# Kernel optimization log

Measured on AMD Instinct MI355X. Metric: run time of the kernel, lower is better.

The kernel has to match this reference:

```python
import jax, jax.numpy as jnp
import numpy as np

N = 50000      # nodes
E = 800000     # edges (before self-loops)
F_IN = 128     # num_node_features
H = 128        # hidden_channels
G = 256        # graphs in batch
T = 4          # num_tasks


def setup_inputs() -> dict:
    key = jax.random.key(0)
    ks = jax.random.split(key, 12)
    x = jax.random.normal(ks[0], (N, F_IN), jnp.float32)
    edge_index = jax.random.randint(ks[1], (2, E), 0, N, dtype=jnp.int64)
    batch = jnp.sort(jax.random.randint(ks[2], (N,), 0, G, dtype=jnp.int64))
    s_in = 1.0 / np.sqrt(F_IN)
    s_h = 1.0 / np.sqrt(H)
    W1 = jax.random.normal(ks[3], (F_IN, H), jnp.float32) * s_in
    b1 = jnp.zeros((H,), jnp.float32)
    W2 = jax.random.normal(ks[4], (H, H), jnp.float32) * s_h
    b2 = jnp.zeros((H,), jnp.float32)
    Wfc = jax.random.normal(ks[5], (H, H), jnp.float32) * s_h
    bfc = jnp.zeros((H,), jnp.float32)
    Wh = jax.random.normal(ks[6], (T, H, 2), jnp.float32) * s_h
    bh = jnp.zeros((T, 2), jnp.float32)
    return {"x": x, "edge_index": edge_index, "batch": batch,
            "W1": W1, "b1": b1, "W2": W2, "b2": b2,
            "Wfc": Wfc, "bfc": bfc, "Wh": Wh, "bh": bh}


def _gcn_layer(x, W, b, src, dst, dinv):
    # GCNConv: out = D^{-1/2}(A+I)D^{-1/2} X W + b  (self-loops already in src/dst)
    h = x @ W                                    # [N, H] dense transform first (fewer edge features)
    coef = dinv[src] * dinv[dst]                 # [E+N] symmetric normalization
    msg = h[src] * coef[:, None]                 # [E+N, H] gathered messages
    out = jax.ops.segment_sum(msg, dst, num_segments=N)
    return out + b


def reference(x, edge_index, batch, W1, b1, W2, b2, Wfc, bfc, Wh, bh):
    loops = jnp.arange(N, dtype=edge_index.dtype)
    src = jnp.concatenate([edge_index[0], loops])  # [E+N]
    dst = jnp.concatenate([edge_index[1], loops])
    deg = jax.ops.segment_sum(jnp.ones_like(dst, dtype=x.dtype), dst, num_segments=N)
    dinv = jax.lax.rsqrt(deg)                      # deg >= 1 due to self-loops

    h = jax.nn.relu(_gcn_layer(x, W1, b1, src, dst, dinv))
    h = jax.nn.relu(_gcn_layer(h, W2, b2, src, dst, dinv))

    # global_mean_pool over batch ids
    sums = jax.ops.segment_sum(h, batch, num_segments=G)          # [G, H]
    cnt = jax.ops.segment_sum(jnp.ones((N,), h.dtype), batch, num_segments=G)
    pooled = sums / jnp.maximum(cnt, 1.0)[:, None]

    z = jax.nn.relu(pooled @ Wfc + bfc)                           # [G, H]
    out = jnp.einsum('gh,thc->tgc', z, Wh) + bh[:, None, :]       # [T, G, 2]
    return out
```

## Files before the change

### kernel.cpp

```cpp
#include <hip/hip_runtime.h>
#include <math.h>

constexpr int N = 50000;
constexpr int E = 800000;
constexpr int F = 128;
constexpr int G = 256;
constexpr int T = 4;

constexpr int BSH   = 5;
constexpr int BNODES= 1 << BSH;
constexpr int NBUCK = (N + BNODES - 1) / BNODES;
constexpr int CHUNK = 2048;
constexpr int NCHUNK= (E + CHUNK - 1) / CHUNK;
constexpr int SSH   = 13;

constexpr int WC_BLKS  = (F * F + 255) / 256;
constexpr int PRE_Z0   = 2 * WC_BLKS;
constexpr int PRE_ZB   = (G * F + 255) / 256;
constexpr int PRE_H0   = PRE_Z0 + PRE_ZB;
constexpr int PRE_BLKS = PRE_H0 + NCHUNK;

constexpr int GB1 = (N + 63) / 64;
constexpr int GCB = GB1 + NBUCK;
constexpr int AGB = N / 16;

typedef __attribute__((ext_vector_type(8))) short short8;
typedef __attribute__((ext_vector_type(4))) float floatx4;

__device__ inline float bf2f(unsigned short u) {
    union { unsigned int i; float f; } v;
    v.i = ((unsigned int)u) << 16;
    return v.f;
}
__device__ inline unsigned short f2bf(float f) {
    union { float f; unsigned int i; } v;
    v.f = f;
    unsigned int r = v.i + 0x7FFF + ((v.i >> 16) & 1);
    return (unsigned short)(r >> 16);
}
__device__ inline unsigned int pack2bf(float a, float b) {
    return (unsigned int)f2bf(a) | ((unsigned int)f2bf(b) << 16);
}

__device__ inline void wcast_one(const float* __restrict__ W,
                                 unsigned short* __restrict__ Whi,
                                 unsigned short* __restrict__ Wlo, int i) {
    if (i >= F * F) return;
    int k = i >> 7, n = i & 127;
    float w = W[i];
    unsigned short hi = f2bf(w);
    unsigned short lo = f2bf(w - bf2f(hi));
    int s = k >> 5, q = (k >> 3) & 3, j = k & 7;
    int idx = (((s * 128 + n) * 4 + q) * 8) + j;
    Whi[idx] = hi;
    Wlo[idx] = lo;
}

__global__ __launch_bounds__(256) void k_pre(const float* __restrict__ W1, const float* __restrict__ W2,
                                             unsigned short* __restrict__ w1h, unsigned short* __restrict__ w1l,
                                             unsigned short* __restrict__ w2h, unsigned short* __restrict__ w2l,
                                             const int* __restrict__ dst, int* __restrict__ cnts,
                                             float* __restrict__ pooled) {
    __shared__ int h[NBUCK];
    int b = blockIdx.x, t = threadIdx.x;
    if (b < WC_BLKS) {
        wcast_one(W1, w1h, w1l, b * 256 + t);
    } else if (b < 2 * WC_BLKS) {
        wcast_one(W2, w2h, w2l, (b - WC_BLKS) * 256 + t);
    } else if (b < PRE_H0) {
        pooled[(b - PRE_Z0) * 256 + t] = 0.f;
    } else {
        int chunk = b - PRE_H0;
        for (int i = t; i < NBUCK; i += 256) h[i] = 0;
        __syncthreads();
        int base = chunk * CHUNK;
        for (int i = t; i < CHUNK; i += 256) {
            int e = base + i;
            if (e < E) atomicAdd(&h[dst[e] >> BSH], 1);
        }
        __syncthreads();
        for (int i = t; i < NBUCK; i += 256) cnts[chunk * NBUCK + i] = h[i];
    }
}

__global__ __launch_bounds__(256) void k_bucketscan(const int* __restrict__ btot,
                                                    int* __restrict__ bucketbase) {
    __shared__ int part[256];
    int t = threadIdx.x;
    constexpr int CH = (NBUCK + 255) / 256;
    int beg = t * CH;
    int end = (beg + CH < NBUCK) ? beg + CH : NBUCK;
    int tot[CH];
    int s = 0;
    for (int i = beg; i < end; ++i) {
        tot[i - beg] = btot[i];
        s += btot[i];
    }
    part[t] = s;
    __syncthreads();
    for (int off = 1; off < 256; off <<= 1) {
        int u = (t >= off) ? part[t - off] : 0;
        __syncthreads();
        part[t] += u;
        __syncthreads();
    }
    int run = (t == 0) ? 0 : part[t - 1];
    for (int i = beg; i < end; ++i) {
        bucketbase[i] = run;
        run += tot[i - beg];
    }
    if (t == 255) bucketbase[NBUCK] = part[255];
}

__global__ __launch_bounds__(256) void k_fillb(const int* __restrict__ src,
                                               const int* __restrict__ dst,
                                               const int* __restrict__ cnts,
                                               const int* __restrict__ bucketbase,
                                               unsigned int* __restrict__ staging) {
    __shared__ int lofs[NBUCK];
    int chunk = blockIdx.x, t = threadIdx.x;
    for (int i = t; i < NBUCK; i += 256)
        lofs[i] = bucketbase[i] + cnts[chunk * NBUCK + i];
    __syncthreads();
    int base = chunk * CHUNK;
    for (int i = t; i < CHUNK; i += 256) {
        int e = base + i;
        if (e < E) {
            int d = dst[e];
            int pos = atomicAdd(&lofs[d >> BSH], 1);
            staging[pos] = (unsigned int)src[e] | ((unsigned int)(d & (BNODES - 1)) << 16);
        }
    }
}

__global__ __launch_bounds__(256) void k_passB(const unsigned int* __restrict__ staging,
                                               const int* __restrict__ bucketbase,
                                               int* __restrict__ csr,
                                               int* __restrict__ rowstart,
                                               float* __restrict__ dinv) {
    __shared__ unsigned int ent[1024];
    __shared__ int h[BNODES * 8], off_a[BNODES * 8];
    __shared__ int nodebase[BNODES], ndeg[BNODES];
    int b = blockIdx.x, t = threadIdx.x;
    int jb = bucketbase[b], je = bucketbase[b + 1];
    int M = je - jb;
    if (M > 1024) M = 1024;
    if (t < BNODES * 8) h[t] = 0;
    __syncthreads();

    for (int i = t; i < M; i += 256) {
        unsigned int en = staging[jb + i];
        ent[i] = en;
        int key = (((en >> 16) & (BNODES - 1)) << 3) | ((en & 0xFFFFu) >> SSH);
        atomicAdd(&h[key], 1);
    }
    __syncthreads();

    if (t < BNODES) {
        int s = 0;
#pragma unroll
        for (int c = 0; c < 8; ++c) s += h[t * 8 + c];
        ndeg[t] = s;
    }
    __syncthreads();
    if (t == 0) {
        int run = jb;
        for (int k = 0; k < BNODES; ++k) {
            nodebase[k] = run;
            run += ndeg[k];
        }
    }
    __syncthreads();
    if (t < BNODES) {
        int run = nodebase[t];
#pragma unroll
        for (int c = 0; c < 8; ++c) {
            off_a[t * 8 + c] = run;
            run += h[t * 8 + c];
        }
        int node = b * BNODES + t;
        if (node < N) {
            rowstart[node] = nodebase[t];
            dinv[node] = rsqrtf((float)(ndeg[t] + 1));
        }
    }
    if (b == 0 && t == 0) rowstart[N] = E;
    __syncthreads();

    for (int i = t; i < M; i += 256) {
        unsigned int en = ent[i];
        int key = (((en >> 16) & (BNODES - 1)) << 3) | ((en & 0xFFFFu) >> SSH);
        int loc = atomicAdd(&off_a[key], 1);
        csr[loc] = (int)(en & 0xFFFFu);
    }
}

template <bool ABF16>
__device__ __forceinline__ void gemm_body(const void* __restrict__ Ain,
                                          const unsigned short* __restrict__ Wph,
                                          const unsigned short* __restrict__ Wpl,
                                          unsigned short* __restrict__ C16,
                                          int row0, int tid,
                                          unsigned short* __restrict__ Albs) {
    if (ABF16) {
        const uint4* A8 = (const uint4*)Ain;
        for (int f = tid; f < 64 * 16; f += 256) {
            int r = f >> 4, kq = f & 15;
            int row = row0 + r;
            uint4 v = make_uint4(0u, 0u, 0u, 0u);
            if (row < N) v = A8[row * 16 + kq];
            *(uint4*)&Albs[r * 136 + kq * 8] = v;
        }
    } else {
        const float4* A4 = (const float4*)Ain;
        for (int f = tid; f < 64 * 32; f += 256) {
            int r = f >> 5, kq = f & 31;
            int row = row0 + r;
            float4 v = make_float4(0.f, 0.f, 0.f, 0.f);
            if (row < N) v = A4[row * 32 + kq];
            ushort4 o;
            o.x = f2bf(v.x); o.y = f2bf(v.y); o.z = f2bf(v.z); o.w = f2bf(v.w);
            *(ushort4*)&Albs[r * 136 + kq * 4] = o;
        }
    }
    __syncthreads();

    int wv = tid >> 6;
    int lane = tid & 63;
    int c16 = lane & 15;
    int q = lane >> 4;
    int m = wv * 16 + c16;

    floatx4 acc[8];
#pragma unroll
    for (int nt = 0; nt < 8; ++nt) acc[nt] = (floatx4){0.f, 0.f, 0.f, 0.f};

    const short8* WH = (const short8*)Wph;
    const short8* WL = (const short8*)Wpl;
#pragma unroll
    for (int s = 0; s < 4; ++s) {
        short8 a = *(const short8*)&Albs[m * 136 + s * 32 + q * 8];
        int wb = s * 512 + c16 * 4 + q;
#pragma unroll
        for (int nt = 0; nt < 8; ++nt) {
            acc[nt] = __builtin_amdgcn_mfma_f32_16x16x32_bf16(a, WH[wb + nt * 64], acc[nt], 0, 0, 0);
            acc[nt] = __builtin_amdgcn_mfma_f32_16x16x32_bf16(a, WL[wb + nt * 64], acc[nt], 0, 0, 0);
        }
    }

    int rbase = row0 + wv * 16 + q * 4;
#pragma unroll
    for (int r = 0; r < 4; ++r) {
        int row = rbase + r;
        if (row < N) {
#pragma unroll
            for (int nt = 0; nt < 8; ++nt)
                C16[row * 128 + nt * 16 + c16] = f2bf(acc[nt][r]);
        }
    }
}

__global__ __launch_bounds__(256) void k_gemmcol(const float* __restrict__ x,
                                                 const unsigned short* __restrict__ w1h,
                                                 const unsigned short* __restrict__ w1l,
                                                 unsigned short* __restrict__ tmp16,
                                                 int* __restrict__ cnts,
                                                 int* __restrict__ btot) {
    __shared__ __align__(16) unsigned short Albs[64 * 136];
    int b = blockIdx.x, t = threadIdx.x;
    if (b < GB1) {
        gemm_body<false>(x, w1h, w1l, tmp16, b * 64, t, Albs);
        return;
    }
    int j = b - GB1;
    int* part = (int*)Albs;
    int k0 = 2 * t, k1 = 2 * t + 1;
    int v0 = (k0 < NCHUNK) ? cnts[k0 * NBUCK + j] : 0;
    int v1 = (k1 < NCHUNK) ? cnts[k1 * NBUCK + j] : 0;
    int s = v0 + v1;
    part[t] = s;
    __syncthreads();
    for (int off = 1; off < 256; off <<= 1) {
        int u = (t >= off) ? part[t - off] : 0;
        __syncthreads();
        part[t] += u;
        __syncthreads();
    }
    int excl = part[t] - s;
    if (k0 < NCHUNK) cnts[k0 * NBUCK + j] = excl;
    if (k1 < NCHUNK) cnts[k1 * NBUCK + j] = excl + v0;
    if (t == 255) btot[j] = part[255];
}

__device__ inline void fma8(const uint4& u, float c, float* acc) {
    union { unsigned int i; float f; } a;
    a.i = u.x << 16;          acc[0] = fmaf(a.f, c, acc[0]);
    a.i = u.x & 0xFFFF0000u;  acc[1] = fmaf(a.f, c, acc[1]);
    a.i = u.y << 16;          acc[2] = fmaf(a.f, c, acc[2]);
    a.i = u.y & 0xFFFF0000u;  acc[3] = fmaf(a.f, c, acc[3]);
    a.i = u.z << 16;          acc[4] = fmaf(a.f, c, acc[4]);
    a.i = u.z & 0xFFFF0000u;  acc[5] = fmaf(a.f, c, acc[5]);
    a.i = u.w << 16;          acc[6] = fmaf(a.f, c, acc[6]);
    a.i = u.w & 0xFFFF0000u;  acc[7] = fmaf(a.f, c, acc[7]);
}

__device__ __forceinline__ void agg_loop(const uint4* __restrict__ t8,
                                         const int* __restrict__ csr,
                                         const float* __restrict__ dinv,
                                         int jb, int je, int lane, float* acc) {
    for (int j = jb; j < je; j += 8) {
        int e[8];
        float cf[8];
#pragma unroll
        for (int k = 0; k < 8; ++k) {
            int idx = j + k;
            e[k] = csr[idx < je ? idx : je - 1];
            cf[k] = (idx < je) ? dinv[e[k]] : 0.0f;
        }
        uint4 u[8];
#pragma unroll
        for (int k = 0; k < 8; ++k) u[k] = t8[e[k] * 16 + lane];
#pragma unroll
        for (int k = 0; k < 8; ++k) fma8(u[k], cf[k], acc);
    }
}

__global__ __launch_bounds__(256) void k_agg1gemm(const unsigned short* __restrict__ tmp16,
                                                  const int* __restrict__ csr,
                                                  const int* __restrict__ rowstart,
                                                  const float* __restrict__ dinv,
                                                  const float* __restrict__ bias,
                                                  const unsigned short* __restrict__ w2h,
                                                  const unsigned short* __restrict__ w2l,
                                                  unsigned short* __restrict__ tmp2) {
    __shared__ __align__(16) unsigned short Albs[16 * 136];
    int tid = threadIdx.x;
    int row0 = blockIdx.x * 16;

    {
        int node = row0 + (tid >> 4);
        int lane = tid & 15;
        const uint4* t8 = (const uint4*)tmp16;
        float di = dinv[node];
        float acc[8] = {0.f, 0.f, 0.f, 0.f, 0.f, 0.f, 0.f, 0.f};
        fma8(t8[node * 16 + lane], di, acc);
        agg_loop(t8, csr, dinv, rowstart[node], rowstart[node + 1], lane, acc);

        const float4* b4 = (const float4*)bias;
        float4 ba = b4[lane * 2], bb = b4[lane * 2 + 1];
        uint4 o;
        o.x = pack2bf(fmaxf(fmaf(acc[0], di, ba.x), 0.f), fmaxf(fmaf(acc[1], di, ba.y), 0.f));
        o.y = pack2bf(fmaxf(fmaf(acc[2], di, ba.z), 0.f), fmaxf(fmaf(acc[3], di, ba.w), 0.f));
        o.z = pack2bf(fmaxf(fmaf(acc[4], di, bb.x), 0.f), fmaxf(fmaf(acc[5], di, bb.y), 0.f));
        o.w = pack2bf(fmaxf(fmaf(acc[6], di, bb.z), 0.f), fmaxf(fmaf(acc[7], di, bb.w), 0.f));
        *(uint4*)&Albs[(tid >> 4) * 136 + lane * 8] = o;
    }
    __syncthreads();

    int wv = tid >> 6;
    int lane = tid & 63;
    int c16 = lane & 15;
    int q = lane >> 4;

    floatx4 acc[2];
    acc[0] = (floatx4){0.f, 0.f, 0.f, 0.f};
    acc[1] = (floatx4){0.f, 0.f, 0.f, 0.f};

    const short8* WH = (const short8*)w2h;
    const short8* WL = (const short8*)w2l;
#pragma unroll
    for (int s = 0; s < 4; ++s) {
        short8 a = *(const short8*)&Albs[c16 * 136 + s * 32 + q * 8];
        int wb = s * 512 + c16 * 4 + q;
#pragma unroll
        for (int i = 0; i < 2; ++i) {
            int nt = wv * 2 + i;
            acc[i] = __builtin_amdgcn_mfma_f32_16x16x32_bf16(a, WH[wb + nt * 64], acc[i], 0, 0, 0);
            acc[i] = __builtin_amdgcn_mfma_f32_16x16x32_bf16(a, WL[wb + nt * 64], acc[i], 0, 0, 0);
        }
    }

    int rbase = row0 + q * 4;
#pragma unroll
    for (int r = 0; r < 4; ++r) {
        int row = rbase + r;
#pragma unroll
        for (int i = 0; i < 2; ++i) {
            int nt = wv * 2 + i;
            tmp2[row * 128 + nt * 16 + c16] = f2bf(acc[i][r]);
        }
    }
}

__global__ __launch_bounds__(256) void k_agg(const unsigned short* __restrict__ tmp16,
                                             const int* __restrict__ csr,
                                             const int* __restrict__ rowstart,
                                             const float* __restrict__ dinv,
                                             const float* __restrict__ bias,
                                             const int* __restrict__ batch,
                                             float* __restrict__ pooled) {
    __shared__ float red[16][128];
    __shared__ int gid[16];
    int tid = threadIdx.x;
    int node0 = blockIdx.x * 16;
    int ns = tid >> 4, lane = tid & 15;
    int node = node0 + ns;
    const uint4* t8 = (const uint4*)tmp16;
    float di = dinv[node];
    float acc[8] = {0.f, 0.f, 0.f, 0.f, 0.f, 0.f, 0.f, 0.f};
    fma8(t8[node * 16 + lane], di, acc);
    agg_loop(t8, csr, dinv, rowstart[node], rowstart[node + 1], lane, acc);

    const float4* b4 = (const float4*)bias;
    float4 ba = b4[lane * 2], bb = b4[lane * 2 + 1];
    red[ns][lane * 8 + 0] = fmaxf(fmaf(acc[0], di, ba.x), 0.f);
    red[ns][lane * 8 + 1] = fmaxf(fmaf(acc[1], di, ba.y), 0.f);
    red[ns][lane * 8 + 2] = fmaxf(fmaf(acc[2], di, ba.z), 0.f);
    red[ns][lane * 8 + 3] = fmaxf(fmaf(acc[3], di, ba.w), 0.f);
    red[ns][lane * 8 + 4] = fmaxf(fmaf(acc[4], di, bb.x), 0.f);
    red[ns][lane * 8 + 5] = fmaxf(fmaf(acc[5], di, bb.y), 0.f);
    red[ns][lane * 8 + 6] = fmaxf(fmaf(acc[6], di, bb.z), 0.f);
    red[ns][lane * 8 + 7] = fmaxf(fmaf(acc[7], di, bb.w), 0.f);
    if (tid < 16) gid[tid] = batch[node0 + tid];
    __syncthreads();

    if (tid < 128) {
        int f = tid;
        float run = 0.f;
        int g = gid[0];
        for (int r = 0; r < 16; ++r) {
            if (gid[r] != g) {
                atomicAdd(&pooled[g * 128 + f], run);
                run = 0.f;
                g = gid[r];
            }
            run += red[r][f];
        }
        atomicAdd(&pooled[g * 128 + f], run);
    }
}

__global__ __launch_bounds__(128) void k_poolhead(const float* __restrict__ pooled,
                                                  const int* __restrict__ batch,
                                                  const float* __restrict__ Wfc,
                                                  const float* __restrict__ bfc,
                                                  const float* __restrict__ Wh,
                                                  const float* __restrict__ bh,
                                                  float* __restrict__ out) {
    __shared__ float p[128];
    __shared__ float zs[128];
    int g = blockIdx.x, t = threadIdx.x;

    int lo = 0, hi = N;
    while (lo < hi) { int m = (lo + hi) >> 1; if (batch[m] < g) lo = m + 1; else hi = m; }
    int lo1 = lo, hi1 = N;
    while (lo1 < hi1) { int m = (lo1 + hi1) >> 1; if (batch[m] < g + 1) lo1 = m + 1; else hi1 = m; }
    int cnt = lo1 - lo;
    float inv = 1.0f / (float)((cnt > 1) ? cnt : 1);

    p[t] = pooled[g * 128 + t] * inv;
    __syncthreads();

    float a = bfc[t];
    for (int k = 0; k < F; ++k) a = fmaf(p[k], Wfc[k * F + t], a);
    zs[t] = fmaxf(a, 0.f);
    __syncthreads();

    if (t < T * 2) {
        int task = t >> 1, c = t & 1;
        float a2 = bh[task * 2 + c];
        const float* wr = &Wh[task * F * 2 + c];
        for (int h = 0; h < F; ++h) a2 = fmaf(zs[h], wr[h * 2], a2);
        out[task * (G * 2) + g * 2 + c] = a2;
    }
}

extern "C" void kernel_launch(void* const* d_in, const int* in_sizes, int n_in,
                              void* d_out, int out_size, void* d_ws, size_t ws_size,
                              hipStream_t stream) {
    const float* x    = (const float*)d_in[0];
    const int*   ei   = (const int*)d_in[1];
    const int*   batch= (const int*)d_in[2];
    const float* W1   = (const float*)d_in[3];
    const float* b1   = (const float*)d_in[4];
    const float* W2   = (const float*)d_in[5];
    const float* b2   = (const float*)d_in[6];
    const float* Wfc  = (const float*)d_in[7];
    const float* bfc  = (const float*)d_in[8];
    const float* Wh   = (const float*)d_in[9];
    const float* bh   = (const float*)d_in[10];
    float* out = (float*)d_out;

    const int* srcp = ei;
    const int* dstp = ei + E;

    char* w = (char*)d_ws;
    auto alloc = [&](size_t bytes) {
        char* p = w;
        w += (bytes + 255) & ~(size_t)255;
        return p;
    };
    unsigned short* tmp16 = (unsigned short*)alloc((size_t)N * F * 2);
    unsigned short* tmp2  = (unsigned short*)alloc((size_t)N * F * 2);
    int*   csr      = (int*)  alloc((size_t)E * 4);
    unsigned int* staging = (unsigned int*)alloc((size_t)E * 4);
    int*   cnts     = (int*)  alloc((size_t)NCHUNK * NBUCK * 4);
    int*   btot     = (int*)  alloc((size_t)NBUCK * 4);
    int*   bucketbase=(int*)  alloc((size_t)(NBUCK + 1) * 4);
    int*   rowstart = (int*)  alloc((size_t)(N + 1) * 4);
    float* dinv     = (float*)alloc((size_t)N * 4);
    float* pooled   = (float*)alloc((size_t)G * F * 4);
    unsigned short* w1h = (unsigned short*)alloc((size_t)F * F * 2);
    unsigned short* w1l = (unsigned short*)alloc((size_t)F * F * 2);
    unsigned short* w2h = (unsigned short*)alloc((size_t)F * F * 2);
    unsigned short* w2l = (unsigned short*)alloc((size_t)F * F * 2);

    k_pre<<<PRE_BLKS, 256, 0, stream>>>(W1, W2, w1h, w1l, w2h, w2l, dstp, cnts, pooled);

    k_gemmcol<<<GCB, 256, 0, stream>>>(x, w1h, w1l, tmp16, cnts, btot);

    k_bucketscan<<<1, 256, 0, stream>>>(btot, bucketbase);
    k_fillb<<<NCHUNK, 256, 0, stream>>>(srcp, dstp, cnts, bucketbase, staging);
    k_passB<<<NBUCK, 256, 0, stream>>>(staging, bucketbase, csr, rowstart, dinv);

    k_agg1gemm<<<AGB, 256, 0, stream>>>(tmp16, csr, rowstart, dinv, b1, w2h, w2l, tmp2);

    k_agg<<<AGB, 256, 0, stream>>>(tmp2, csr, rowstart, dinv, b2, batch, pooled);

    k_poolhead<<<G, 128, 0, stream>>>(pooled, batch, Wfc, bfc, Wh, bh, out);
}
```

Before: 232.0 us.

## Prescale GEMM outputs by dinv, fuse bucket scan into fill, pipeline CSR loads

Per-node in-degree is now counted with global atomics in the pre-pass. That lets dinv be computed inside the first GEMM epilogue, and each transformed row is stored already multiplied by dinv[src]. The aggregation loops then sum rows with plain adds instead of gathering dinv per edge, and the second GEMM likewise prescales its output. The single-block bucket scan kernel is folded into every fill block, removing one launch at the cost of redundant scans. The aggregation loop also prefetches the next group of CSR indices. The new global atomics and memset add some cost.

```diff
diff --git a/kernel.cpp b/kernel.cpp
--- a/kernel.cpp
+++ b/kernel.cpp
@@ -60,7 +60,7 @@
                                              unsigned short* __restrict__ w1h, unsigned short* __restrict__ w1l,
                                              unsigned short* __restrict__ w2h, unsigned short* __restrict__ w2l,
                                              const int* __restrict__ dst, int* __restrict__ cnts,
-                                             float* __restrict__ pooled) {
+                                             float* __restrict__ pooled, int* __restrict__ ndeg) {
     __shared__ int h[NBUCK];
     int b = blockIdx.x, t = threadIdx.x;
     if (b < WC_BLKS) {
@@ -76,17 +76,28 @@
         int base = chunk * CHUNK;
         for (int i = t; i < CHUNK; i += 256) {
             int e = base + i;
-            if (e < E) atomicAdd(&h[dst[e] >> BSH], 1);
+            if (e < E) {
+                int d = dst[e];
+                atomicAdd(&h[d >> BSH], 1);
+                atomicAdd(&ndeg[d], 1);
+            }
         }
         __syncthreads();
         for (int i = t; i < NBUCK; i += 256) cnts[chunk * NBUCK + i] = h[i];
     }
 }
 
-__global__ __launch_bounds__(256) void k_bucketscan(const int* __restrict__ btot,
-                                                    int* __restrict__ bucketbase) {
+__global__ __launch_bounds__(256) void k_fillb(const int* __restrict__ src,
+                                               const int* __restrict__ dst,
+                                               const int* __restrict__ cnts,
+                                               const int* __restrict__ btot,
+                                               int* __restrict__ bucketbase,
+                                               unsigned int* __restrict__ staging) {
+    __shared__ int bb[NBUCK + 1];
     __shared__ int part[256];
-    int t = threadIdx.x;
+    __shared__ int lofs[NBUCK];
+    int chunk = blockIdx.x, t = threadIdx.x;
+
     constexpr int CH = (NBUCK + 255) / 256;
     int beg = t * CH;
     int end = (beg + CH < NBUCK) ? beg + CH : NBUCK;
@@ -106,22 +117,18 @@
     }
     int run = (t == 0) ? 0 : part[t - 1];
     for (int i = beg; i < end; ++i) {
-        bucketbase[i] = run;
+        bb[i] = run;
         run += tot[i - beg];
     }
-    if (t == 255) bucketbase[NBUCK] = part[255];
-}
-
-__global__ __launch_bounds__(256) void k_fillb(const int* __restrict__ src,
-                                               const int* __restrict__ dst,
-                                               const int* __restrict__ cnts,
-                                               const int* __restrict__ bucketbase,
-                                               unsigned int* __restrict__ staging) {
-    __shared__ int lofs[NBUCK];
-    int chunk = blockIdx.x, t = threadIdx.x;
+    if (t == 255) bb[NBUCK] = part[255];
+    __syncthreads();
+    if (chunk == 0)
+        for (int i = t; i <= NBUCK; i += 256) bucketbase[i] = bb[i];
+
     for (int i = t; i < NBUCK; i += 256)
-        lofs[i] = bucketbase[i] + cnts[chunk * NBUCK + i];
-    __syncthreads();
+        lofs[i] = bb[i] + cnts[chunk * NBUCK + i];
+    __syncthreads();
+
     int base = chunk * CHUNK;
     for (int i = t; i < CHUNK; i += 256) {
         int e = base + i;
@@ -136,8 +143,7 @@
 __global__ __launch_bounds__(256) void k_passB(const unsigned int* __restrict__ staging,
                                                const int* __restrict__ bucketbase,
                                                int* __restrict__ csr,
-                                               int* __restrict__ rowstart,
-                                               float* __restrict__ dinv) {
+                                               int* __restrict__ rowstart) {
     __shared__ unsigned int ent[1024];
     __shared__ int h[BNODES * 8], off_a[BNODES * 8];
     __shared__ int nodebase[BNODES], ndeg[BNODES];
@@ -179,10 +185,7 @@
             run += h[t * 8 + c];
         }
         int node = b * BNODES + t;
-        if (node < N) {
-            rowstart[node] = nodebase[t];
-            dinv[node] = rsqrtf((float)(ndeg[t] + 1));
-        }
+        if (node < N) rowstart[node] = nodebase[t];
     }
     if (b == 0 && t == 0) rowstart[N] = E;
     __syncthreads();
@@ -199,6 +202,8 @@
 __device__ __forceinline__ void gemm_body(const void* __restrict__ Ain,
                                           const unsigned short* __restrict__ Wph,
                                           const unsigned short* __restrict__ Wpl,
+                                          const int* __restrict__ ndeg,
+                                          float* __restrict__ dinvout,
                                           unsigned short* __restrict__ C16,
                                           int row0, int tid,
                                           unsigned short* __restrict__ Albs) {
@@ -253,9 +258,11 @@
     for (int r = 0; r < 4; ++r) {
         int row = rbase + r;
         if (row < N) {
+            float dv = rsqrtf((float)(ndeg[row] + 1));
+            if (c16 == 0) dinvout[row] = dv;
 #pragma unroll
             for (int nt = 0; nt < 8; ++nt)
-                C16[row * 128 + nt * 16 + c16] = f2bf(acc[nt][r]);
+                C16[row * 128 + nt * 16 + c16] = f2bf(acc[nt][r] * dv);
         }
     }
 }
@@ -263,13 +270,15 @@
 __global__ __launch_bounds__(256) void k_gemmcol(const float* __restrict__ x,
                                                  const unsigned short* __restrict__ w1h,
                                                  const unsigned short* __restrict__ w1l,
+                                                 const int* __restrict__ ndeg,
+                                                 float* __restrict__ dinv,
                                                  unsigned short* __restrict__ tmp16,
                                                  int* __restrict__ cnts,
                                                  int* __restrict__ btot) {
     __shared__ __align__(16) unsigned short Albs[64 * 136];
     int b = blockIdx.x, t = threadIdx.x;
     if (b < GB1) {
-        gemm_body<false>(x, w1h, w1l, tmp16, b * 64, t, Albs);
+        gemm_body<false>(x, w1h, w1l, ndeg, dinv, tmp16, b * 64, t, Albs);
         return;
     }
     int j = b - GB1;
@@ -290,6 +299,18 @@
     if (k0 < NCHUNK) cnts[k0 * NBUCK + j] = excl;
     if (k1 < NCHUNK) cnts[k1 * NBUCK + j] = excl + v0;
     if (t == 255) btot[j] = part[255];
+}
+
+__device__ inline void add8(const uint4& u, float* acc) {
+    union { unsigned int i; float f; } a;
+    a.i = u.x << 16;          acc[0] += a.f;
+    a.i = u.x & 0xFFFF0000u;  acc[1] += a.f;
+    a.i = u.y << 16;          acc[2] += a.f;
+    a.i = u.y & 0xFFFF0000u;  acc[3] += a.f;
+    a.i = u.z << 16;          acc[4] += a.f;
+    a.i = u.z & 0xFFFF0000u;  acc[5] += a.f;
+    a.i = u.w << 16;          acc[6] += a.f;
+    a.i = u.w & 0xFFFF0000u;  acc[7] += a.f;
 }
 
 __device__ inline void fma8(const uint4& u, float c, float* acc) {
@@ -304,24 +325,42 @@
     a.i = u.w & 0xFFFF0000u;  acc[7] = fmaf(a.f, c, acc[7]);
 }
 
-__device__ __forceinline__ void agg_loop(const uint4* __restrict__ t8,
+__device__ __forceinline__ void agg_loop(const uint4* __restrict__ t8l,
                                          const int* __restrict__ csr,
-                                         const float* __restrict__ dinv,
-                                         int jb, int je, int lane, float* acc) {
-    for (int j = jb; j < je; j += 8) {
+                                         int jb, int je, float* acc) {
+    int n8 = (je - jb) >> 3;
+    int j = jb;
+    if (n8 > 0) {
         int e[8];
-        float cf[8];
+#pragma unroll
+        for (int k = 0; k < 8; ++k) e[k] = csr[j + k];
+        for (int c = 0; c < n8; ++c) {
+            uint4 u[8];
+#pragma unroll
+            for (int k = 0; k < 8; ++k) u[k] = t8l[e[k] * 16];
+            j += 8;
+            if (c + 1 < n8) {
+#pragma unroll
+                for (int k = 0; k < 8; ++k) e[k] = csr[j + k];
+            }
+#pragma unroll
+            for (int k = 0; k < 8; ++k) add8(u[k], acc);
+        }
+    }
+    if (j < je) {
+        int e[8];
+        float msk[8];
 #pragma unroll
         for (int k = 0; k < 8; ++k) {
             int idx = j + k;
             e[k] = csr[idx < je ? idx : je - 1];
-            cf[k] = (idx < je) ? dinv[e[k]] : 0.0f;
+            msk[k] = (idx < je) ? 1.0f : 0.0f;
         }
         uint4 u[8];
 #pragma unroll
-        for (int k = 0; k < 8; ++k) u[k] = t8[e[k] * 16 + lane];
-#pragma unroll
-        for (int k = 0; k < 8; ++k) fma8(u[k], cf[k], acc);
+        for (int k = 0; k < 8; ++k) u[k] = t8l[e[k] * 16];
+#pragma unroll
+        for (int k = 0; k < 8; ++k) fma8(u[k], msk[k], acc);
     }
 }
 
@@ -340,12 +379,12 @@
     {
         int node = row0 + (tid >> 4);
         int lane = tid & 15;
-        const uint4* t8 = (const uint4*)tmp16;
+        const uint4* t8l = (const uint4*)tmp16 + lane;
+        float acc[8] = {0.f, 0.f, 0.f, 0.f, 0.f, 0.f, 0.f, 0.f};
+        add8(t8l[node * 16], acc);
+        agg_loop(t8l, csr, rowstart[node], rowstart[node + 1], acc);
+
         float di = dinv[node];
-        float acc[8] = {0.f, 0.f, 0.f, 0.f, 0.f, 0.f, 0.f, 0.f};
-        fma8(t8[node * 16 + lane], di, acc);
-        agg_loop(t8, csr, dinv, rowstart[node], rowstart[node + 1], lane, acc);
-
         const float4* b4 = (const float4*)bias;
         float4 ba = b4[lane * 2], bb = b4[lane * 2 + 1];
         uint4 o;
@@ -384,10 +423,11 @@
 #pragma unroll
     for (int r = 0; r < 4; ++r) {
         int row = rbase + r;
+        float dv = dinv[row];
 #pragma unroll
         for (int i = 0; i < 2; ++i) {
             int nt = wv * 2 + i;
-            tmp2[row * 128 + nt * 16 + c16] = f2bf(acc[i][r]);
+            tmp2[row * 128 + nt * 16 + c16] = f2bf(acc[i][r] * dv);
         }
     }
 }
@@ -405,12 +445,12 @@
     int node0 = blockIdx.x * 16;
     int ns = tid >> 4, lane = tid & 15;
     int node = node0 + ns;
-    const uint4* t8 = (const uint4*)tmp16;
+    const uint4* t8l = (const uint4*)tmp16 + lane;
+    float acc[8] = {0.f, 0.f, 0.f, 0.f, 0.f, 0.f, 0.f, 0.f};
+    add8(t8l[node * 16], acc);
+    agg_loop(t8l, csr, rowstart[node], rowstart[node + 1], acc);
+
     float di = dinv[node];
-    float acc[8] = {0.f, 0.f, 0.f, 0.f, 0.f, 0.f, 0.f, 0.f};
-    fma8(t8[node * 16 + lane], di, acc);
-    agg_loop(t8, csr, dinv, rowstart[node], rowstart[node + 1], lane, acc);
-
     const float4* b4 = (const float4*)bias;
     float4 ba = b4[lane * 2], bb = b4[lane * 2 + 1];
     red[ns][lane * 8 + 0] = fmaxf(fmaf(acc[0], di, ba.x), 0.f);
@@ -508,6 +548,7 @@
     int*   btot     = (int*)  alloc((size_t)NBUCK * 4);
     int*   bucketbase=(int*)  alloc((size_t)(NBUCK + 1) * 4);
     int*   rowstart = (int*)  alloc((size_t)(N + 1) * 4);
+    int*   ndeg     = (int*)  alloc((size_t)N * 4);
     float* dinv     = (float*)alloc((size_t)N * 4);
     float* pooled   = (float*)alloc((size_t)G * F * 4);
     unsigned short* w1h = (unsigned short*)alloc((size_t)F * F * 2);
@@ -515,13 +556,14 @@
     unsigned short* w2h = (unsigned short*)alloc((size_t)F * F * 2);
     unsigned short* w2l = (unsigned short*)alloc((size_t)F * F * 2);
 
-    k_pre<<<PRE_BLKS, 256, 0, stream>>>(W1, W2, w1h, w1l, w2h, w2l, dstp, cnts, pooled);
-
-    k_gemmcol<<<GCB, 256, 0, stream>>>(x, w1h, w1l, tmp16, cnts, btot);
-
-    k_bucketscan<<<1, 256, 0, stream>>>(btot, bucketbase);
-    k_fillb<<<NCHUNK, 256, 0, stream>>>(srcp, dstp, cnts, bucketbase, staging);
-    k_passB<<<NBUCK, 256, 0, stream>>>(staging, bucketbase, csr, rowstart, dinv);
+    hipMemsetAsync(ndeg, 0, (size_t)N * 4, stream);
+
+    k_pre<<<PRE_BLKS, 256, 0, stream>>>(W1, W2, w1h, w1l, w2h, w2l, dstp, cnts, pooled, ndeg);
+
+    k_gemmcol<<<GCB, 256, 0, stream>>>(x, w1h, w1l, ndeg, dinv, tmp16, cnts, btot);
+
+    k_fillb<<<NCHUNK, 256, 0, stream>>>(srcp, dstp, cnts, btot, bucketbase, staging);
+    k_passB<<<NBUCK, 256, 0, stream>>>(staging, bucketbase, csr, rowstart);
 
     k_agg1gemm<<<AGB, 256, 0, stream>>>(tmp16, csr, rowstart, dinv, b1, w2h, w2l, tmp2);
 
```

Result: slower. 244.2 us (+5.3%).
